# Optimization experiments

Measured on AMD Instinct MI355X. Metric: run time of the kernel, lower is better.

## Reference

```python
import jax, jax.numpy as jnp
import numpy as np

S, B, I, H = 512, 64, 512, 1024  # seq_len, batch, input_size, hidden_size


def setup_inputs() -> dict:
    key = jax.random.key(0)
    k0, k1, k2, k3, k4 = jax.random.split(key, 5)
    x = jax.random.normal(k0, (S, B, I), dtype=jnp.float32)
    # nn.Linear-style init scale
    Ww = jax.random.uniform(k1, (H, H), jnp.float32, -1.0, 1.0) / np.float32(np.sqrt(H))
    Wb = jax.random.uniform(k2, (H,), jnp.float32, -1.0, 1.0) / np.float32(np.sqrt(H))
    Vw = jax.random.uniform(k3, (H, I), jnp.float32, -1.0, 1.0) / np.float32(np.sqrt(I))
    Vb = jax.random.uniform(k4, (H,), jnp.float32, -1.0, 1.0) / np.float32(np.sqrt(I))
    return {"x": x, "Ww": Ww, "Wb": Wb, "Vw": Vw, "Vb": Vb}


def reference(x, Ww, Wb, Vw, Vb):
    # h_t = tanh(W h_{t-1} + b_W + V x_t + b_V); h_0 = 0
    # Input projection has no temporal dependence -> one big batched matmul.
    Vx = jnp.einsum('sbi,hi->sbh', x, Vw) + Vb  # (S, B, H)

    def step(h, vx_t):
        h = jnp.tanh(h @ Ww.T + Wb + vx_t)
        return h, h

    h0 = jnp.zeros((x.shape[1], Ww.shape[0]), dtype=x.dtype)
    h_final, h_seq = jax.lax.scan(step, h0, Vx)
    # torch code cats the (1,B,H)-broadcast hidden states along dim 0 -> (S,B,H),
    # and returns the final hidden as (1,B,H).
    return h_seq, h_final[None]
```

## Files before the change

kernel.cpp:

```cpp
#include <hip/hip_runtime.h>
#include <math.h>

#define RS 512
#define RB 64
#define RI 512
#define RH 1024

#define NG   8
#define WPG  32
#define BPG  8

__global__ __launch_bounds__(256) void vx_gemm(const float* __restrict__ A,
                                               const float* __restrict__ W,
                                               const float* __restrict__ bias,
                                               float* __restrict__ C,
                                               int M, int N, int K) {
    __shared__ __align__(16) float As[16][68];
    __shared__ __align__(16) float Bs[16][68];

    const int tx = threadIdx.x;
    const int ty = threadIdx.y;
    const int tid = ty * 16 + tx;
    const int m0 = blockIdx.y * 64;
    const int n0 = blockIdx.x * 64;

    float acc[4][4] = {};

    const int row  = tid >> 2;
    const int quad = tid & 3;

    for (int k0 = 0; k0 < K; k0 += 16) {
        float4 av = *(const float4*)&A[(size_t)(m0 + row) * K + k0 + quad * 4];
        float4 wv = *(const float4*)&W[(size_t)(n0 + row) * K + k0 + quad * 4];
        const int kq = quad * 4;
        As[kq + 0][row] = av.x; As[kq + 1][row] = av.y;
        As[kq + 2][row] = av.z; As[kq + 3][row] = av.w;
        Bs[kq + 0][row] = wv.x; Bs[kq + 1][row] = wv.y;
        Bs[kq + 2][row] = wv.z; Bs[kq + 3][row] = wv.w;
        __syncthreads();

        #pragma unroll
        for (int k = 0; k < 16; ++k) {
            float4 a = *(const float4*)&As[k][ty * 4];
            float4 b = *(const float4*)&Bs[k][tx * 4];
            float am[4] = {a.x, a.y, a.z, a.w};
            float bn[4] = {b.x, b.y, b.z, b.w};
            #pragma unroll
            for (int i = 0; i < 4; ++i)
                #pragma unroll
                for (int j = 0; j < 4; ++j)
                    acc[i][j] = fmaf(am[i], bn[j], acc[i][j]);
        }
        __syncthreads();
    }

    #pragma unroll
    for (int i = 0; i < 4; ++i) {
        const int m = m0 + ty * 4 + i;
        const int n = n0 + tx * 4;
        float4 o;
        o.x = acc[i][0] + bias[n + 0];
        o.y = acc[i][1] + bias[n + 1];
        o.z = acc[i][2] + bias[n + 2];
        o.w = acc[i][3] + bias[n + 3];
        *(float4*)&C[(size_t)m * N + n] = o;
    }
}

__global__ __launch_bounds__(256, 1) void rnn_persistent(
    const float* __restrict__ Ww, const float* __restrict__ Wb,
    float* __restrict__ hseq, float* __restrict__ hfin,
    float* __restrict__ hex, int* __restrict__ flags)
{
    const int tid  = threadIdx.x;
    const int wgid = blockIdx.x;
    const int g    = wgid & 7;
    const int sub  = wgid >> 3;
    const int j0   = sub * 32;
    const int b0   = g * BPG;

    const int wave = tid >> 6, lane = tid & 63;
    const int kc = wave * 4 + (lane >> 4);
    const int jp = lane & 15;

    const int o_jl = tid & 31, o_bl = tid >> 5;
    const int oj = j0 + o_jl;

    float wreg[2][64];
    {
        const float* base = Ww + (size_t)(j0 + jp * 2) * RH + kc * 64;
        #pragma unroll
        for (int jj = 0; jj < 2; ++jj)
            #pragma unroll
            for (int ki = 0; ki < 64; ki += 4) {
                float4 v = *(const float4*)(base + (size_t)jj * RH + ki);
                wreg[jj][ki + 0] = v.x; wreg[jj][ki + 1] = v.y;
                wreg[jj][ki + 2] = v.z; wreg[jj][ki + 3] = v.w;
            }
    }
    const float wb = Wb[oj];

    __shared__ __align__(16) float Hs[8256];
    __shared__ __align__(16) float Red[4096];

    int* gflags = flags + g * WPG;

    for (int t = 0; t < RS; ++t) {
        float acc[16];
        #pragma unroll
        for (int i = 0; i < 16; ++i) acc[i] = 0.f;

        if (t > 0) {
            const unsigned long long* src = (const unsigned long long*)
                (hex + ((size_t)((t - 1) & 1) * NG + g) * (RH * BPG));
            #pragma unroll
            for (int i = 0; i < 16; ++i) {
                const int idx = tid + 256 * i;
                unsigned long long u = __hip_atomic_load(src + idx,
                    __ATOMIC_RELAXED, __HIP_MEMORY_SCOPE_AGENT);
                union { unsigned long long u; float f[2]; } cv; cv.u = u;
                const int k = idx >> 2, q = idx & 3;
                const int base = k * 8 + (k >> 6) * 4 + q * 2;
                Hs[base] = cv.f[0]; Hs[base + 1] = cv.f[1];
            }
            __syncthreads();

            const float4* hv = (const float4*)Hs;
            const int hbase = kc * 129;
            #pragma unroll
            for (int ki = 0; ki < 64; ++ki) {
                const float4 h0 = hv[hbase + ki * 2];
                const float4 h1 = hv[hbase + ki * 2 + 1];
                const float w0 = wreg[0][ki], w1 = wreg[1][ki];
                acc[0]  = fmaf(w0, h0.x, acc[0]);  acc[1]  = fmaf(w0, h0.y, acc[1]);
                acc[2]  = fmaf(w0, h0.z, acc[2]);  acc[3]  = fmaf(w0, h0.w, acc[3]);
                acc[4]  = fmaf(w0, h1.x, acc[4]);  acc[5]  = fmaf(w0, h1.y, acc[5]);
                acc[6]  = fmaf(w0, h1.z, acc[6]);  acc[7]  = fmaf(w0, h1.w, acc[7]);
                acc[8]  = fmaf(w1, h0.x, acc[8]);  acc[9]  = fmaf(w1, h0.y, acc[9]);
                acc[10] = fmaf(w1, h0.z, acc[10]); acc[11] = fmaf(w1, h0.w, acc[11]);
                acc[12] = fmaf(w1, h1.x, acc[12]); acc[13] = fmaf(w1, h1.y, acc[13]);
                acc[14] = fmaf(w1, h1.z, acc[14]); acc[15] = fmaf(w1, h1.w, acc[15]);
            }

            float4* rp = (float4*)&Red[(kc * 16 + jp) * 16];
            rp[0] = make_float4(acc[0],  acc[1],  acc[2],  acc[3]);
            rp[1] = make_float4(acc[4],  acc[5],  acc[6],  acc[7]);
            rp[2] = make_float4(acc[8],  acc[9],  acc[10], acc[11]);
            rp[3] = make_float4(acc[12], acc[13], acc[14], acc[15]);
            __syncthreads();
        }

        float z = 0.f;
        if (t > 0) {
            const int rbase = (o_jl >> 1) * 16 + (o_jl & 1) * 8 + o_bl;
            #pragma unroll
            for (int kk = 0; kk < 16; ++kk)
                z += Red[kk * 256 + rbase];
        }
        float* cell = hseq + (size_t)t * (RB * RH) + (size_t)(b0 + o_bl) * RH + oj;
        const float h = tanhf(z + wb + *cell);
        *cell = h;

        if (t == RS - 1) {
            hfin[(size_t)(b0 + o_bl) * RH + oj] = h;
        } else {
            __hip_atomic_store(
                hex + ((size_t)(t & 1) * NG + g) * (RH * BPG) + (size_t)oj * BPG + o_bl,
                h, __ATOMIC_RELAXED, __HIP_MEMORY_SCOPE_AGENT);
            __syncthreads();
            if (tid == 0)
                __hip_atomic_store(&gflags[sub], t + 1,
                                   __ATOMIC_RELEASE, __HIP_MEMORY_SCOPE_AGENT);
            if (wave == 0) {
                const int target = t + 1;
                const int idx = lane & 31;
                while (__hip_atomic_load(&gflags[idx], __ATOMIC_RELAXED,
                                         __HIP_MEMORY_SCOPE_AGENT) < target) {}
            }
            __syncthreads();
        }
    }
}

extern "C" void kernel_launch(void* const* d_in, const int* in_sizes, int n_in,
                              void* d_out, int out_size, void* d_ws, size_t ws_size,
                              hipStream_t stream) {
    const float* x  = (const float*)d_in[0];
    const float* Ww = (const float*)d_in[1];
    const float* Wb = (const float*)d_in[2];
    const float* Vw = (const float*)d_in[3];
    const float* Vb = (const float*)d_in[4];

    float* out  = (float*)d_out;
    float* hseq = out;
    float* hfin = out + (size_t)RS * RB * RH;

    int*   flags = (int*)d_ws;
    float* hex   = (float*)((char*)d_ws + 1024);

    {
        dim3 grid(RH / 64, (RS * RB) / 64);
        dim3 block(16, 16);
        vx_gemm<<<grid, block, 0, stream>>>(x, Vw, Vb, hseq, RS * RB, RH, RI);
    }

    rnn_persistent<<<dim3(NG * WPG), dim3(256), 0, stream>>>(Ww, Wb, hseq, hfin,
                                                             hex, flags);
}
```

Measured before the change: 7.846 ms.

## Group recurrent workgroups by XCD and use L2-scoped loads for hidden-state exchange

Each workgroup reads its hardware XCD id and publishes it, then all workgroups agree on a remap. If the XCDs are evenly populated, each batch group of 32 workgroups is placed on a single XCD. In that fast mode, the per-step hidden-state exchange and flag polling use sc0 global loads and volatile stores instead of agent-scope atomics, so traffic stays in the shared L2 rather than going device-wide. The flag wait also moves to the start of the next step, the Vx prefetch is hoisted, and the reduction buffer is padded against bank conflicts. This relies on weaker memory ordering without explicit fences, and adds an xcds workspace array that is never reset between launches.

Measured after the change: 8.116 ms. +3.4%, slower.

```diff
diff --git a/kernel.cpp b/kernel.cpp
--- a/kernel.cpp
+++ b/kernel.cpp
@@ -9,6 +9,8 @@
 #define NG   8
 #define WPG  32
 #define BPG  8
+
+typedef float f32x4 __attribute__((ext_vector_type(4)));
 
 __global__ __launch_bounds__(256) void vx_gemm(const float* __restrict__ A,
                                                const float* __restrict__ W,
@@ -70,19 +72,53 @@
 __global__ __launch_bounds__(256, 1) void rnn_persistent(
     const float* __restrict__ Ww, const float* __restrict__ Wb,
     float* __restrict__ hseq, float* __restrict__ hfin,
-    float* __restrict__ hex, int* __restrict__ flags)
+    float* __restrict__ hex, int* __restrict__ flags, int* __restrict__ xcds)
 {
+    __shared__ __align__(16) float Hs[8256];
+    __shared__ __align__(16) float Red[16 * 272];
+    __shared__ int sx[256];
+    __shared__ int s_info;
+
     const int tid  = threadIdx.x;
     const int wgid = blockIdx.x;
-    const int g    = wgid & 7;
-    const int sub  = wgid >> 3;
+    const int wave = tid >> 6, lane = tid & 63;
+
+    if (tid == 0) {
+        const int x = (int)(__builtin_amdgcn_s_getreg(6164) & 7u);
+        __hip_atomic_store(&xcds[wgid], x + 1, __ATOMIC_RELEASE,
+                           __HIP_MEMORY_SCOPE_AGENT);
+    }
+    {
+        int v;
+        do {
+            v = __hip_atomic_load(&xcds[tid], __ATOMIC_RELAXED,
+                                  __HIP_MEMORY_SCOPE_AGENT);
+        } while (v == 0);
+        sx[tid] = v - 1;
+    }
+    __syncthreads();
+    if (tid == 0) {
+        int cnt[8] = {};
+        for (int w = 0; w < 256; ++w) cnt[sx[w] & 7]++;
+        bool uni = true;
+        for (int i = 0; i < 8; ++i) uni = uni && (cnt[i] == 32);
+        int rank = 0;
+        const int mine = sx[wgid];
+        for (int w = 0; w < wgid; ++w) rank += (sx[w] == mine);
+        int g, slot;
+        if (uni) { g = mine & 7;  slot = rank; }
+        else     { g = wgid & 7;  slot = wgid >> 3; }
+        s_info = (uni ? 0x10000 : 0) | (g << 8) | slot;
+    }
+    __syncthreads();
+    const int fast = (s_info >> 16) & 1;
+    const int g    = (s_info >> 8) & 7;
+    const int sub  = s_info & 0xff;
     const int j0   = sub * 32;
     const int b0   = g * BPG;
 
-    const int wave = tid >> 6, lane = tid & 63;
     const int kc = wave * 4 + (lane >> 4);
     const int jp = lane & 15;
-
     const int o_jl = tid & 31, o_bl = tid >> 5;
     const int oj = j0 + o_jl;
 
@@ -100,37 +136,72 @@
     }
     const float wb = Wb[oj];
 
-    __shared__ __align__(16) float Hs[8256];
-    __shared__ __align__(16) float Red[4096];
-
     int* gflags = flags + g * WPG;
 
     for (int t = 0; t < RS; ++t) {
-        float acc[16];
-        #pragma unroll
-        for (int i = 0; i < 16; ++i) acc[i] = 0.f;
-
+        float* cell = hseq + (size_t)t * (RB * RH) + (size_t)(b0 + o_bl) * RH + oj;
+        const float vx = *cell;
+
+        float red = 0.f;
         if (t > 0) {
-            const unsigned long long* src = (const unsigned long long*)
-                (hex + ((size_t)((t - 1) & 1) * NG + g) * (RH * BPG));
-            #pragma unroll
-            for (int i = 0; i < 16; ++i) {
-                const int idx = tid + 256 * i;
-                unsigned long long u = __hip_atomic_load(src + idx,
-                    __ATOMIC_RELAXED, __HIP_MEMORY_SCOPE_AGENT);
-                union { unsigned long long u; float f[2]; } cv; cv.u = u;
-                const int k = idx >> 2, q = idx & 3;
-                const int base = k * 8 + (k >> 6) * 4 + q * 2;
-                Hs[base] = cv.f[0]; Hs[base + 1] = cv.f[1];
-            }
-            __syncthreads();
-
-            const float4* hv = (const float4*)Hs;
+            if (wave == 0) {
+                const int* fp = gflags + (lane & 31);
+                if (fast) {
+                    int f;
+                    do {
+                        asm volatile("global_load_dword %0, %1, off sc0\n\t"
+                                     "s_waitcnt vmcnt(0)"
+                                     : "=v"(f) : "v"(fp) : "memory");
+                    } while (f < t);
+                } else {
+                    while (__hip_atomic_load(fp, __ATOMIC_RELAXED,
+                                             __HIP_MEMORY_SCOPE_AGENT) < t) {}
+                }
+            }
+            __syncthreads();
+
+            const float* srcf = hex + ((size_t)((t - 1) & 1) * NG + g) * (RH * BPG);
+            if (fast) {
+                const f32x4* src = (const f32x4*)srcf;
+                f32x4 r0, r1, r2, r3, r4, r5, r6, r7;
+#define LDX(i, r) asm volatile("global_load_dwordx4 %0, %1, off sc0" \
+                               : "=v"(r) : "v"(src + (tid + 256 * i)))
+                LDX(0, r0); LDX(1, r1); LDX(2, r2); LDX(3, r3);
+                LDX(4, r4); LDX(5, r5); LDX(6, r6); LDX(7, r7);
+#undef LDX
+                asm volatile("s_waitcnt vmcnt(0)"
+                             : "+v"(r0), "+v"(r1), "+v"(r2), "+v"(r3),
+                               "+v"(r4), "+v"(r5), "+v"(r6), "+v"(r7));
+#define STX(i, r) { const int idx4 = tid + 256 * i; const int k = idx4 >> 1; \
+                    *(f32x4*)&Hs[k * 8 + (k >> 6) * 4 + (idx4 & 1) * 4] = r; }
+                STX(0, r0); STX(1, r1); STX(2, r2); STX(3, r3);
+                STX(4, r4); STX(5, r5); STX(6, r6); STX(7, r7);
+#undef STX
+            } else {
+                const unsigned long long* src = (const unsigned long long*)srcf;
+                #pragma unroll
+                for (int i = 0; i < 16; ++i) {
+                    const int idx = tid + 256 * i;
+                    unsigned long long u = __hip_atomic_load(src + idx,
+                        __ATOMIC_RELAXED, __HIP_MEMORY_SCOPE_AGENT);
+                    union { unsigned long long u; float f[2]; } cv; cv.u = u;
+                    const int k = idx >> 2, q = idx & 3;
+                    const int base = k * 8 + (k >> 6) * 4 + q * 2;
+                    Hs[base] = cv.f[0]; Hs[base + 1] = cv.f[1];
+                }
+            }
+            __syncthreads();
+
+            float acc[16];
+            #pragma unroll
+            for (int i = 0; i < 16; ++i) acc[i] = 0.f;
+
+            const f32x4* hv = (const f32x4*)Hs;
             const int hbase = kc * 129;
             #pragma unroll
             for (int ki = 0; ki < 64; ++ki) {
-                const float4 h0 = hv[hbase + ki * 2];
-                const float4 h1 = hv[hbase + ki * 2 + 1];
+                const f32x4 h0 = hv[hbase + ki * 2];
+                const f32x4 h1 = hv[hbase + ki * 2 + 1];
                 const float w0 = wreg[0][ki], w1 = wreg[1][ki];
                 acc[0]  = fmaf(w0, h0.x, acc[0]);  acc[1]  = fmaf(w0, h0.y, acc[1]);
                 acc[2]  = fmaf(w0, h0.z, acc[2]);  acc[3]  = fmaf(w0, h0.w, acc[3]);
@@ -142,42 +213,37 @@
                 acc[14] = fmaf(w1, h1.z, acc[14]); acc[15] = fmaf(w1, h1.w, acc[15]);
             }
 
-            float4* rp = (float4*)&Red[(kc * 16 + jp) * 16];
-            rp[0] = make_float4(acc[0],  acc[1],  acc[2],  acc[3]);
-            rp[1] = make_float4(acc[4],  acc[5],  acc[6],  acc[7]);
-            rp[2] = make_float4(acc[8],  acc[9],  acc[10], acc[11]);
-            rp[3] = make_float4(acc[12], acc[13], acc[14], acc[15]);
-            __syncthreads();
+            float* rp = Red + tid;
+            #pragma unroll
+            for (int v = 0; v < 16; ++v) rp[v * 272] = acc[v];
+            __syncthreads();
+
+            const int vb = ((o_jl & 1) * 8 + o_bl) * 272 + (o_jl >> 1);
+            #pragma unroll
+            for (int kk = 0; kk < 16; ++kk) red += Red[vb + kk * 16];
         }
 
-        float z = 0.f;
-        if (t > 0) {
-            const int rbase = (o_jl >> 1) * 16 + (o_jl & 1) * 8 + o_bl;
-            #pragma unroll
-            for (int kk = 0; kk < 16; ++kk)
-                z += Red[kk * 256 + rbase];
-        }
-        float* cell = hseq + (size_t)t * (RB * RH) + (size_t)(b0 + o_bl) * RH + oj;
-        const float h = tanhf(z + wb + *cell);
-        *cell = h;
-
-        if (t == RS - 1) {
+        const float h = tanhf(red + wb + vx);
+
+        if (t < RS - 1) {
+            float* dst = hex + ((size_t)(t & 1) * NG + g) * (RH * BPG)
+                             + (size_t)oj * BPG + o_bl;
+            if (fast) {
+                *(volatile float*)dst = h;
+            } else {
+                __hip_atomic_store(dst, h, __ATOMIC_RELAXED,
+                                   __HIP_MEMORY_SCOPE_AGENT);
+            }
+            __syncthreads();
+            if (tid == 0) {
+                if (fast) ((volatile int*)gflags)[sub] = t + 1;
+                else __hip_atomic_store(&gflags[sub], t + 1, __ATOMIC_RELEASE,
+                                        __HIP_MEMORY_SCOPE_AGENT);
+            }
+            *cell = h;
+        } else {
+            *cell = h;
             hfin[(size_t)(b0 + o_bl) * RH + oj] = h;
-        } else {
-            __hip_atomic_store(
-                hex + ((size_t)(t & 1) * NG + g) * (RH * BPG) + (size_t)oj * BPG + o_bl,
-                h, __ATOMIC_RELAXED, __HIP_MEMORY_SCOPE_AGENT);
-            __syncthreads();
-            if (tid == 0)
-                __hip_atomic_store(&gflags[sub], t + 1,
-                                   __ATOMIC_RELEASE, __HIP_MEMORY_SCOPE_AGENT);
-            if (wave == 0) {
-                const int target = t + 1;
-                const int idx = lane & 31;
-                while (__hip_atomic_load(&gflags[idx], __ATOMIC_RELAXED,
-                                         __HIP_MEMORY_SCOPE_AGENT) < target) {}
-            }
-            __syncthreads();
         }
     }
 }
@@ -196,7 +262,8 @@
     float* hfin = out + (size_t)RS * RB * RH;
 
     int*   flags = (int*)d_ws;
-    float* hex   = (float*)((char*)d_ws + 1024);
+    int*   xcds  = (int*)((char*)d_ws + 1024);
+    float* hex   = (float*)((char*)d_ws + 2048);
 
     {
         dim3 grid(RH / 64, (RS * RB) / 64);
@@ -205,5 +272,5 @@
     }
 
     rnn_persistent<<<dim3(NG * WPG), dim3(256), 0, stream>>>(Ww, Wb, hseq, hfin,
-                                                             hex, flags);
+                                                             hex, flags, xcds);
 }
```
